# Optimization experiments

Hardware: AMD Instinct MI355X
Metric: run time of the kernel (lower is better)

## Reference

```python
import jax, jax.numpy as jnp
import numpy as np

C = 256            # in_channels
SHIFTS = (1, 2, 3, 4)
S = len(SHIFTS)
HID = C // S       # 64
H = W = 64
AREA = H * W
EPS = 1e-5
NORM_EPS = 1e-12
# offsets (dy, dx) encoded by the 8 one-hot 3x3 kernels (kernels 1..8)
OFFSETS = [(-1,-1), (-1,0), (-1,1), (0,1), (1,1), (1,0), (1,-1), (0,-1)]


def shift2d(x, dy, dx):
    # x: [b, c, H, W]; out[y, x] = x[y+dy, x+dx], zeros outside (== dilated depthwise conv with one-hot kernel)
    d = max(abs(dy), abs(dx), 1)
    xp = jnp.pad(x, ((0,0),(0,0),(d,d),(d,d)))
    return xp[:, :, d+dy:d+dy+x.shape[2], d+dx:d+dx+x.shape[3]]


def setup_inputs() -> dict:
    key = jax.random.key(0)
    ks = jax.random.split(key, 8)
    sd = 0.02
    return {
        "cen": jax.random.normal(ks[0], (4, C, H, W), dtype=jnp.float32),
        "query_w": jax.random.normal(ks[1], (S, HID, C), dtype=jnp.float32) * sd,
        "local_w": jax.random.normal(ks[2], (S, HID, C), dtype=jnp.float32) * sd,
        "key_w":   jax.random.normal(ks[3], (S, 8*HID, 8*C), dtype=jnp.float32) * sd,
        "value_w": jax.random.normal(ks[4], (S, 8*HID, 8*C), dtype=jnp.float32) * sd,
        "out_w":   jax.random.normal(ks[5], (C, C), dtype=jnp.float32) * sd,
        "bn_gamma": jnp.ones((C,), dtype=jnp.float32),
        "bn_beta":  jnp.zeros((C,), dtype=jnp.float32),
    }


def reference(cen, query_w, local_w, key_w, value_w, out_w, bn_gamma, bn_beta):
    b, _, h, w = cen.shape
    cenf = cen.reshape(b, C, AREA)
    keys, qs, vals, locs = [], [], [], []
    for i, d in enumerate(SHIFTS):
        # gather 8 dilated neighbors -> [b, 8C, area]
        surr = jnp.concatenate([shift2d(cen, dy*d, dx*d) for dy, dx in OFFSETS], axis=1)
        surr = surr.reshape(b, 8*C, AREA)
        keys.append(jnp.einsum('oc,bca->boa', key_w[i], surr))
        vals.append(jnp.einsum('oc,bca->boa', value_w[i], surr))
        qs.append(jnp.einsum('oc,bca->boa', query_w[i], cenf))
        locs.append(jnp.einsum('oc,bca->boa', local_w[i], cenf))
    keys = jnp.stack(keys, 1)   # [b,S,8h,area]
    vals = jnp.stack(vals, 1)   # [b,S,8h,area]
    qs   = jnp.stack(qs, 1)     # [b,S,h,area]
    locs = jnp.stack(locs, 1)   # [b,S,h,area]

    # L2 normalize over area (torch F.normalize: x / max(||x||, eps))
    kn = keys / jnp.maximum(jnp.linalg.norm(keys, axis=-1, keepdims=True), NORM_EPS)
    qn = qs   / jnp.maximum(jnp.linalg.norm(qs,   axis=-1, keepdims=True), NORM_EPS)

    # channel attention: contract over area -> [b,S,h,8h]
    score = jnp.einsum('bsha,bska->bshk', qn, kn)
    # InstanceNorm2d over (h, 8h) per (b, S), affine=False, biased var
    mu = score.mean(axis=(-2,-1), keepdims=True)
    var = score.var(axis=(-2,-1), keepdims=True)
    score = (score - mu) * jax.lax.rsqrt(var + EPS)
    ws = jax.nn.softmax(score, axis=-1)                     # [b,S,h,8h]
    wc = ws.reshape(b, S, HID, 8, HID).sum(axis=3)          # sum of 8 chunks -> [b,S,h,h]

    out = jnp.einsum('bshk,bska->bsha', ws, vals) - jnp.einsum('bshk,bska->bsha', wc, locs)
    out = out.reshape(b, C, h, w)

    # out_conv: 1x1 conv -> BatchNorm2d (training stats, biased var) -> ReLU
    out = jnp.einsum('oc,bchw->bohw', out_w, out)
    m = out.mean(axis=(0,2,3), keepdims=True)
    v = out.var(axis=(0,2,3), keepdims=True)
    out = (out - m) * jax.lax.rsqrt(v + EPS)
    out = out * bn_gamma[None, :, None, None] + bn_beta[None, :, None, None]
    return jax.nn.relu(out)
```

## Files before the change

kernel.cpp:

```cpp
#include <hip/hip_runtime.h>


typedef unsigned short u16;
typedef unsigned int u32;
typedef __attribute__((ext_vector_type(4))) unsigned int u32x4;
typedef __attribute__((ext_vector_type(8))) short s16x8;
typedef __attribute__((ext_vector_type(4))) float f32x4;

#define DEVFN static __device__ __forceinline__

DEVFN u16 f2bf(float f) {
    u32 u = __builtin_bit_cast(u32, f);
    u32 r = (u + 0x7fffu + ((u >> 16) & 1u)) >> 16;
    return (u16)r;
}
DEVFN float bf2f(u32 h) { u32 u = h << 16; return __builtin_bit_cast(float, u); }

typedef __attribute__((address_space(1))) const unsigned int gu32;
typedef __attribute__((address_space(3))) unsigned int lu32;
DEVFN void gld16(const void* g, void* l) {
    __builtin_amdgcn_global_load_lds((gu32*)g, (lu32*)l, 16, 0, 0);
}

__constant__ int cOFFY[8] = {-1,-1,-1, 0, 1, 1, 1, 0};
__constant__ int cOFFX[8] = {-1, 0, 1, 1, 1, 0,-1,-1};

DEVFN int swz(int r, int kb) { return r * 128 + (kb ^ ((r & 7) << 4)); }

template<int BM, int BN, int WRM, int WRN, int XG, int YG, int DM, int NRM>
__global__ __launch_bounds__(256, 2)
void gemm_tn(const u16* __restrict__ X, const u16* __restrict__ Y,
             void* __restrict__ D, const u16* __restrict__ cenT,
             const char* __restrict__ zeroPg, float* __restrict__ nrm,
             int K, int ldx, int ldy, int ldd, int sbits,
             long xb, long xs, long yb, long ys, long db, long dsn,
             long nb, long ns)
{
    const int tid  = threadIdx.x;
    const int lane = tid & 63;
    const int wid  = tid >> 6;
    const int z = blockIdx.z;
    const int b = z >> sbits;
    const int s = z & ((1 << sbits) - 1);
    const int m0 = blockIdx.x * BM;
    const int n0 = blockIdx.y * BN;
    const int dil = s + 1;
    const int wm0 = (wid >> 1) * (WRM * 16);
    const int wn0 = (wid & 1) * (WRN * 16);

    __shared__ __align__(16) char lds[2 * (BM + BN) * 128];

    const char* cenB = (const char*)(cenT + (long)b * (4096 * 256));
    const char* Xb = nullptr;
    const char* Yb = nullptr;
    if constexpr (!XG) Xb = (const char*)(X + b * xb + (long)s * xs + (long)m0 * ldx);
    if constexpr (!YG) Yb = (const char*)(Y + b * yb + (long)s * ys + (long)n0 * ldy);

    auto stage = [&](int bf, int t) {
        char* LX = lds + bf * ((BM + BN) * 128);
        char* LY = LX + BM * 128;
        if constexpr (!XG) {
            const char* base = Xb + (long)t * 128;
            #pragma unroll
            for (int r = 0; r < BM / 32; r++) {
                const int R = r * 32 + wid * 8 + (lane >> 3);
                gld16(base + (long)R * (ldx * 2) + (((lane & 7) * 16) ^ ((R & 7) << 4)),
                      LX + (r * 32 + wid * 8) * 128);
            }
        } else {
            const int j = t >> 2;
            const int dy = (j < 8) ? cOFFY[j] * dil : 0;
            const int dx = (j < 8) ? cOFFX[j] * dil : 0;
            const int cb = (t & 3) * 128;
            #pragma unroll
            for (int r = 0; r < BM / 32; r++) {
                const int R = r * 32 + wid * 8 + (lane >> 3);
                const int a = m0 + R, yy = (a >> 6) + dy, xx = (a & 63) + dx;
                const int off = ((lane & 7) * 16) ^ ((R & 7) << 4);
                const char* src = (((unsigned)yy < 64u) && ((unsigned)xx < 64u))
                    ? cenB + ((long)((yy << 6) + xx) << 9) + cb + off
                    : zeroPg + off;
                gld16(src, LX + (r * 32 + wid * 8) * 128);
            }
        }
        if constexpr (!YG) {
            const char* base = Yb + (long)t * 128;
            #pragma unroll
            for (int r = 0; r < BN / 32; r++) {
                const int R = r * 32 + wid * 8 + (lane >> 3);
                gld16(base + (long)R * (ldy * 2) + (((lane & 7) * 16) ^ ((R & 7) << 4)),
                      LY + (r * 32 + wid * 8) * 128);
            }
        } else {
            const int j = t >> 2;
            const int dy = (j < 8) ? cOFFY[j] * dil : 0;
            const int dx = (j < 8) ? cOFFX[j] * dil : 0;
            const int cb = (t & 3) * 128;
            #pragma unroll
            for (int r = 0; r < BN / 32; r++) {
                const int R = r * 32 + wid * 8 + (lane >> 3);
                const int a = n0 + R, yy = (a >> 6) + dy, xx = (a & 63) + dx;
                const int off = ((lane & 7) * 16) ^ ((R & 7) << 4);
                const char* src = (((unsigned)yy < 64u) && ((unsigned)xx < 64u))
                    ? cenB + ((long)((yy << 6) + xx) << 9) + cb + off
                    : zeroPg + off;
                gld16(src, LY + (r * 32 + wid * 8) * 128);
            }
        }
    };

    f32x4 acc[WRM][WRN] = {};

    auto comp = [&](int bf) {
        const char* LX = lds + bf * ((BM + BN) * 128);
        const char* LY = LX + BM * 128;
        #pragma unroll
        for (int kk = 0; kk < 2; kk++) {
            const int kb = kk * 64 + ((lane >> 4) << 4);
            s16x8 af[WRM], bfr[WRN];
            #pragma unroll
            for (int m = 0; m < WRM; m++)
                af[m] = *(const s16x8*)(LX + swz(wm0 + m * 16 + (lane & 15), kb));
            #pragma unroll
            for (int n = 0; n < WRN; n++)
                bfr[n] = *(const s16x8*)(LY + swz(wn0 + n * 16 + (lane & 15), kb));
            #pragma unroll
            for (int m = 0; m < WRM; m++)
                #pragma unroll
                for (int n = 0; n < WRN; n++)
                    acc[m][n] = __builtin_amdgcn_mfma_f32_16x16x32_bf16(af[m], bfr[n], acc[m][n], 0, 0, 0);
        }
    };

    const int nt = K / 64;
    stage(0, 0);
    __syncthreads();
    int cur = 0;
    for (int t = 0; t < nt; t++) {
        if (t + 1 < nt) stage(cur ^ 1, t + 1);
        comp(cur);
        __syncthreads();
        cur ^= 1;
    }

    if constexpr (NRM) {
        const int slot = (blockIdx.y << 1) + (wid & 1);
        #pragma unroll
        for (int m = 0; m < WRM; m++) {
            float ss[4] = {0.f, 0.f, 0.f, 0.f};
            float s1v[4] = {0.f, 0.f, 0.f, 0.f};
            #pragma unroll
            for (int n = 0; n < WRN; n++)
                #pragma unroll
                for (int i = 0; i < 4; i++) {
                    float v = (NRM == 1) ? bf2f(f2bf(acc[m][n][i])) : acc[m][n][i];
                    ss[i] += v * v;
                    if constexpr (NRM == 2) s1v[i] += v;
                }
            #pragma unroll
            for (int o = 1; o < 16; o <<= 1)
                #pragma unroll
                for (int i = 0; i < 4; i++) {
                    ss[i] += __shfl_xor(ss[i], o);
                    if constexpr (NRM == 2) s1v[i] += __shfl_xor(s1v[i], o);
                }
            if ((lane & 15) == 0) {
                const int row0 = m0 + wm0 + m * 16 + ((lane >> 4) << 2);
                #pragma unroll
                for (int i = 0; i < 4; i++) {
                    if constexpr (NRM == 1) {
                        nrm[((long)(b * nb + s * ns + row0 + i) << 6) + slot] = ss[i];
                    } else {
                        float* p = nrm + ((long)(row0 + i) << 8) + (b << 6) + slot;
                        p[0] = s1v[i];
                        p[65536] = ss[i];
                    }
                }
            }
        }
    }

    #pragma unroll
    for (int m = 0; m < WRM; m++) {
        const int row0 = m0 + wm0 + m * 16 + ((lane >> 4) << 2);
        #pragma unroll
        for (int n = 0; n < WRN; n++) {
            const int col = n0 + wn0 + n * 16 + (lane & 15);
            f32x4 a = acc[m][n];
            if constexpr (DM == 1) {
                float* Dp = (float*)D + b * db + (long)s * dsn;
                #pragma unroll
                for (int i = 0; i < 4; i++) Dp[(long)(row0 + i) * ldd + col] = a[i];
            } else {
                u16* Dp = (u16*)D + b * db + (long)s * dsn;
                #pragma unroll
                for (int i = 0; i < 4; i++) Dp[(long)(row0 + i) * ldd + col] = f2bf(a[i]);
            }
        }
    }
}

__global__ __launch_bounds__(256) void zero_f32(float* __restrict__ p, int n) {
    int i = blockIdx.x * 256 + threadIdx.x;
    if (i < n) p[i] = 0.f;
}

__global__ void castbf(const float* __restrict__ src, u16* __restrict__ dst, int n8, float scale) {
    int i = blockIdx.x * 256 + threadIdx.x;
    if (i >= n8) return;
    const float* s = src + (long)i * 8;
    u32x4 o;
    #pragma unroll
    for (int j = 0; j < 4; j++) {
        u16 lo = f2bf(s[2 * j] * scale), hi = f2bf(s[2 * j + 1] * scale);
        o[j] = (u32)lo | ((u32)hi << 16);
    }
    *(u32x4*)(dst + (long)i * 8) = o;
}

__global__ __launch_bounds__(256) void transpose_cast(const float* __restrict__ src, u16* __restrict__ dst,
                                                      int R, int C, float scale) {
    __shared__ float t[64][65];
    const int tx = threadIdx.x & 63, ty = threadIdx.x >> 6;
    const int c0 = blockIdx.x * 64, r0 = blockIdx.y * 64;
    const long bb = (long)blockIdx.z * R * C;
    const float* s = src + bb + (long)r0 * C + c0;
    #pragma unroll
    for (int i = 0; i < 16; i++) t[ty + i * 4][tx] = s[(long)(ty + i * 4) * C + tx];
    __syncthreads();
    u16* d = dst + bb + (long)c0 * R + r0;
    #pragma unroll
    for (int i = 0; i < 16; i++) d[(long)(ty + i * 4) * R + tx] = f2bf(t[tx][ty + i * 4] * scale);
}

__global__ __launch_bounds__(256) void softmax_in(const float* __restrict__ score,
                                                  const float* __restrict__ nQp,
                                                  const float* __restrict__ nKp,
                                                  u16* __restrict__ wswc) {
    const int bs = blockIdx.x, tid = threadIdx.x;
    const int b = bs >> 2, s = bs & 3;
    const float* S = score + (long)bs * 32768;
    __shared__ float invq[64], invk[512];
    if (tid < 64) {
        const float* p = nQp + ((long)(b * 256 + s * 64 + tid) << 6);
        float a = 0.f;
        #pragma unroll
        for (int j = 0; j < 64; j++) a += p[j];
        invq[tid] = 1.f / fmaxf(sqrtf(a), 1e-12f);
    }
    for (int i = tid; i < 512; i += 256) {
        const float* p = nKp + (((long)bs * 512 + i) << 6);
        float a = 0.f;
        #pragma unroll
        for (int j = 0; j < 64; j++) a += p[j];
        invk[i] = 1.f / fmaxf(sqrtf(a), 1e-12f);
    }
    __syncthreads();
    float s1 = 0.f, s2 = 0.f;
    for (int i = tid; i < 32768; i += 256) {
        float v = S[i] * invq[i >> 9] * invk[i & 511];
        s1 += v; s2 += v * v;
    }
    __shared__ float ra[256], rb[256];
    ra[tid] = s1; rb[tid] = s2; __syncthreads();
    for (int st = 128; st > 0; st >>= 1) {
        if (tid < st) { ra[tid] += ra[tid + st]; rb[tid] += rb[tid + st]; }
        __syncthreads();
    }
    const float mu = ra[0] * (1.f / 32768.f);
    const float var = rb[0] * (1.f / 32768.f) - mu * mu;
    const float rstd = rsqrtf(var + 1e-5f);
    const int wid = tid >> 6, lane = tid & 63;
    u16* W = wswc + (long)bs * 64 * 576;
    for (int r = wid; r < 64; r += 4) {
        float zv[8]; float mx = -3.0e38f;
        const float iq = invq[r];
        #pragma unroll
        for (int i = 0; i < 8; i++) {
            const int c = i * 64 + lane;
            zv[i] = (S[r * 512 + c] * iq * invk[c] - mu) * rstd;
            mx = fmaxf(mx, zv[i]);
        }
        #pragma unroll
        for (int o = 32; o > 0; o >>= 1) mx = fmaxf(mx, __shfl_xor(mx, o));
        float sum = 0.f;
        #pragma unroll
        for (int i = 0; i < 8; i++) { zv[i] = __expf(zv[i] - mx); sum += zv[i]; }
        #pragma unroll
        for (int o = 32; o > 0; o >>= 1) sum += __shfl_xor(sum, o);
        const float inv = 1.f / sum;
        float wcv = 0.f;
        #pragma unroll
        for (int i = 0; i < 8; i++) {
            float w = zv[i] * inv; wcv += w;
            W[r * 576 + i * 64 + lane] = f2bf(w);
        }
        W[r * 576 + 512 + lane] = f2bf(wcv);
    }
}

__global__ __launch_bounds__(256) void bn_finalize(const float* __restrict__ bnp,
                                                   const float* __restrict__ gamma,
                                                   const float* __restrict__ beta,
                                                   float* __restrict__ st) {
    const int c = threadIdx.x;
    const float* p = bnp + ((long)c << 8);
    float s1 = 0.f, s2 = 0.f;
    #pragma unroll 8
    for (int j = 0; j < 256; j++) { s1 += p[j]; s2 += p[65536 + j]; }
    const float mu = s1 * (1.f / 16384.f);
    const float var = s2 * (1.f / 16384.f) - mu * mu;
    const float g = gamma[c] * rsqrtf(var + 1e-5f);
    st[c * 2] = g;
    st[c * 2 + 1] = beta[c] - mu * g;
}

__global__ __launch_bounds__(256) void bn_apply(const u16* __restrict__ out2b,
                                                const float* __restrict__ st,
                                                float* __restrict__ out) {
    const long i8 = (long)blockIdx.x * 256 + threadIdx.x;
    const u32x4 v = *(const u32x4*)(out2b + i8 * 8);
    const int c = (int)((i8 * 8) >> 12) & 255;
    const float g = st[c * 2], bt = st[c * 2 + 1];
    float* o = out + i8 * 8;
    #pragma unroll
    for (int j = 0; j < 4; j++) {
        o[2 * j]     = fmaxf(bf2f(v[j] & 0xffff) * g + bt, 0.f);
        o[2 * j + 1] = fmaxf(bf2f(v[j] >> 16) * g + bt, 0.f);
    }
}

extern "C" void kernel_launch(void* const* d_in, const int* in_sizes, int n_in,
                              void* d_out, int out_size, void* d_ws, size_t ws_size,
                              hipStream_t stream) {
    (void)in_sizes; (void)n_in; (void)out_size; (void)ws_size;
    const float* cen   = (const float*)d_in[0];
    const float* qw    = (const float*)d_in[1];
    const float* lw    = (const float*)d_in[2];
    const float* kw    = (const float*)d_in[3];
    const float* vw    = (const float*)d_in[4];
    const float* ow    = (const float*)d_in[5];
    const float* gamma = (const float*)d_in[6];
    const float* beta  = (const float*)d_in[7];
    float* out = (float*)d_out;

    char* ws = (char*)d_ws;
    size_t off = 0;
    auto alloc = [&](size_t bytes) { size_t o = off; off += (bytes + 255) & ~(size_t)255; return o; };
    u16*   KWb   = (u16*)(ws + alloc(4L * 512 * 2048 * 2));
    u16*   VWt   = (u16*)(ws + alloc(4L * 2048 * 512 * 2));
    u16*   QWb   = (u16*)(ws + alloc(256L * 256 * 2));
    u16*   LWt   = (u16*)(ws + alloc(4L * 256 * 64 * 2));
    u16*   OWb   = (u16*)(ws + alloc(256L * 256 * 2));
    u16*   cenT  = (u16*)(ws + alloc(4L * 4096 * 256 * 2));
    u16*   keys  = (u16*)(ws + alloc(16L * 512 * 4096 * 2));
    u16*   qs    = (u16*)(ws + alloc(16L * 64 * 4096 * 2));
    float* score = (float*)(ws + alloc(16L * 64 * 512 * 4));
    u16*   WSWC  = (u16*)(ws + alloc(16L * 64 * 576 * 2));
    u16*   Xcomb = (u16*)(ws + alloc(16L * 64 * 2304 * 2));
    u16*   out1t = (u16*)(ws + alloc(4L * 4096 * 256 * 2));
    u16*   out2b = (u16*)(ws + alloc(4L * 256 * 4096 * 2));
    float* bnst  = (float*)(ws + alloc(256L * 2 * 4));
    char*  zpg   = (char*)(ws + alloc(256));
    float* nKp   = (float*)(ws + alloc(16L * 512 * 64 * 4));
    float* nQp   = (float*)(ws + alloc(4L * 256 * 64 * 4));
    float* bnp   = (float*)(ws + alloc(2L * 65536 * 4));

    zero_f32<<<dim3(1), 256, 0, stream>>>((float*)zpg, 64);
    castbf<<<dim3(2048), 256, 0, stream>>>(kw, KWb, 524288, 1.f);
    castbf<<<dim3(32),   256, 0, stream>>>(qw, QWb, 8192, 1.f);
    castbf<<<dim3(32),   256, 0, stream>>>(ow, OWb, 8192, 1.f);
    transpose_cast<<<dim3(32, 8, 4), 256, 0, stream>>>(vw, VWt, 512, 2048, 1.f);
    transpose_cast<<<dim3(4, 1, 4),  256, 0, stream>>>(lw, LWt, 64, 256, -1.f);
    transpose_cast<<<dim3(64, 4, 4), 256, 0, stream>>>(cen, cenT, 256, 4096, 1.f);

    gemm_tn<128,128,4,4, 0,1, 0, 1><<<dim3(4, 32, 16), 256, 0, stream>>>(
        KWb, nullptr, keys, cenT, zpg, nKp,
        2048, 2048, 0, 4096, 2,
        0L, 512L * 2048, 0L, 0L, 4L * 512 * 4096, 512L * 4096, 2048L, 512L);
    gemm_tn<128,128,4,4, 0,0, 0, 1><<<dim3(2, 32, 4), 256, 0, stream>>>(
        QWb, cenT, qs, cenT, zpg, nQp,
        256, 256, 256, 4096, 0,
        0L, 0L, 4096L * 256, 0L, 256L * 4096, 0L, 256L, 0L);
    gemm_tn<64,64,2,2, 0,0, 1, 0><<<dim3(1, 8, 16), 256, 0, stream>>>(
        qs, keys, score, cenT, zpg, nullptr,
        4096, 4096, 4096, 512, 2,
        256L * 4096, 64L * 4096, 4L * 512 * 4096, 512L * 4096, 4L * 64 * 512, 64L * 512, 0L, 0L);
    softmax_in<<<dim3(16), 256, 0, stream>>>(score, nQp, nKp, WSWC);

    gemm_tn<64,128,2,4, 0,0, 0, 0><<<dim3(1, 16, 16), 256, 0, stream>>>(
        WSWC, VWt, Xcomb, cenT, zpg, nullptr,
        512, 576, 512, 2304, 2,
        4L * 64 * 576, 64L * 576, 0L, 2048L * 512, 4L * 64 * 2304, 64L * 2304, 0L, 0L);
    gemm_tn<64,128,2,4, 0,0, 0, 0><<<dim3(1, 2, 16), 256, 0, stream>>>(
        WSWC + 512, LWt, Xcomb + 2048, cenT, zpg, nullptr,
        64, 576, 64, 2304, 2,
        4L * 64 * 576, 64L * 576, 0L, 256L * 64, 4L * 64 * 2304, 64L * 2304, 0L, 0L);
    gemm_tn<128,64,4,2, 1,0, 0, 0><<<dim3(32, 1, 16), 256, 0, stream>>>(
        nullptr, Xcomb, out1t, cenT, zpg, nullptr,
        2304, 0, 2304, 256, 2,
        0L, 0L, 4L * 64 * 2304, 64L * 2304, 4096L * 256, 64L, 0L, 0L);

    gemm_tn<128,128,4,4, 0,0, 0, 2><<<dim3(2, 32, 4), 256, 0, stream>>>(
        OWb, out1t, out2b, cenT, zpg, bnp,
        256, 256, 256, 4096, 0,
        0L, 0L, 4096L * 256, 0L, 256L * 4096, 0L, 0L, 0L);

    bn_finalize<<<dim3(1), 256, 0, stream>>>(bnp, gamma, beta, bnst);
    bn_apply<<<dim3(2048), 256, 0, stream>>>(out2b, bnst, out);
}
```

Baseline: 340.1 us.

## Add BK=32 tile path for key GEMM and split-K for score GEMM

Adds a BK=32 K-tile variant of the GEMM with its own LDS swizzle and launch bounds allowing four blocks per SM, and uses it for the large gathered key projection to raise occupancy. Adds split-K (4 slices) to the qs·keys score GEMM, which previously launched only 128 blocks over a 4096-long reduction. Each split writes its own partial plane, and the softmax kernel sums the four partials on load. This trades more partial-score traffic and a larger workspace for better GPU fill on the score GEMM. The K-loop also runs twice as many iterations with more syncs for the key GEMM.

```diff
diff --git a/kernel.cpp b/kernel.cpp
--- a/kernel.cpp
+++ b/kernel.cpp
@@ -27,15 +27,17 @@
 
 DEVFN int swz(int r, int kb) { return r * 128 + (kb ^ ((r & 7) << 4)); }
 
-template<int BM, int BN, int WRM, int WRN, int XG, int YG, int DM, int NRM>
-__global__ __launch_bounds__(256, 2)
+template<int BM, int BN, int WRM, int WRN, int XG, int YG, int DM, int NRM, int BK, int KSP>
+__global__ __launch_bounds__(256, (BK == 32 ? 4 : 2))
 void gemm_tn(const u16* __restrict__ X, const u16* __restrict__ Y,
              void* __restrict__ D, const u16* __restrict__ cenT,
              const char* __restrict__ zeroPg, float* __restrict__ nrm,
              int K, int ldx, int ldy, int ldd, int sbits,
              long xb, long xs, long yb, long ys, long db, long dsn,
-             long nb, long ns)
+             long nb, long ns, long kpl)
 {
+    static_assert(KSP == 1 || (!XG && !YG), "split-K only for non-gather");
+    constexpr int ROWB = BK * 2;
     const int tid  = threadIdx.x;
     const int lane = tid & 63;
     const int wid  = tid >> 6;
@@ -43,87 +45,149 @@
     const int b = z >> sbits;
     const int s = z & ((1 << sbits) - 1);
     const int m0 = blockIdx.x * BM;
-    const int n0 = blockIdx.y * BN;
+    const int ksl = (KSP > 1) ? ((int)blockIdx.y % KSP) : 0;
+    const int n0 = (KSP > 1 ? ((int)blockIdx.y / KSP) : (int)blockIdx.y) * BN;
+    const int koff = ksl * (K / KSP);
     const int dil = s + 1;
     const int wm0 = (wid >> 1) * (WRM * 16);
     const int wn0 = (wid & 1) * (WRN * 16);
 
-    __shared__ __align__(16) char lds[2 * (BM + BN) * 128];
+    __shared__ __align__(16) char lds[2 * (BM + BN) * ROWB];
 
     const char* cenB = (const char*)(cenT + (long)b * (4096 * 256));
     const char* Xb = nullptr;
     const char* Yb = nullptr;
-    if constexpr (!XG) Xb = (const char*)(X + b * xb + (long)s * xs + (long)m0 * ldx);
-    if constexpr (!YG) Yb = (const char*)(Y + b * yb + (long)s * ys + (long)n0 * ldy);
+    if constexpr (!XG) Xb = (const char*)(X + b * xb + (long)s * xs + (long)m0 * ldx + koff);
+    if constexpr (!YG) Yb = (const char*)(Y + b * yb + (long)s * ys + (long)n0 * ldy + koff);
 
     auto stage = [&](int bf, int t) {
-        char* LX = lds + bf * ((BM + BN) * 128);
-        char* LY = LX + BM * 128;
-        if constexpr (!XG) {
-            const char* base = Xb + (long)t * 128;
-            #pragma unroll
-            for (int r = 0; r < BM / 32; r++) {
-                const int R = r * 32 + wid * 8 + (lane >> 3);
-                gld16(base + (long)R * (ldx * 2) + (((lane & 7) * 16) ^ ((R & 7) << 4)),
-                      LX + (r * 32 + wid * 8) * 128);
+        char* LX = lds + bf * ((BM + BN) * ROWB);
+        char* LY = LX + BM * ROWB;
+        if constexpr (BK == 64) {
+            if constexpr (!XG) {
+                const char* base = Xb + (long)t * 128;
+                #pragma unroll
+                for (int r = 0; r < BM / 32; r++) {
+                    const int R = r * 32 + wid * 8 + (lane >> 3);
+                    gld16(base + (long)R * (ldx * 2) + (((lane & 7) * 16) ^ ((R & 7) << 4)),
+                          LX + (r * 32 + wid * 8) * 128);
+                }
+            } else {
+                const int j = t >> 2;
+                const int dy = (j < 8) ? cOFFY[j] * dil : 0;
+                const int dx = (j < 8) ? cOFFX[j] * dil : 0;
+                const int cb = (t & 3) * 128;
+                #pragma unroll
+                for (int r = 0; r < BM / 32; r++) {
+                    const int R = r * 32 + wid * 8 + (lane >> 3);
+                    const int a = m0 + R, yy = (a >> 6) + dy, xx = (a & 63) + dx;
+                    const int off = ((lane & 7) * 16) ^ ((R & 7) << 4);
+                    const char* src = (((unsigned)yy < 64u) && ((unsigned)xx < 64u))
+                        ? cenB + ((long)((yy << 6) + xx) << 9) + cb + off
+                        : zeroPg + off;
+                    gld16(src, LX + (r * 32 + wid * 8) * 128);
+                }
+            }
+            if constexpr (!YG) {
+                const char* base = Yb + (long)t * 128;
+                #pragma unroll
+                for (int r = 0; r < BN / 32; r++) {
+                    const int R = r * 32 + wid * 8 + (lane >> 3);
+                    gld16(base + (long)R * (ldy * 2) + (((lane & 7) * 16) ^ ((R & 7) << 4)),
+                          LY + (r * 32 + wid * 8) * 128);
+                }
+            } else {
+                const int j = t >> 2;
+                const int dy = (j < 8) ? cOFFY[j] * dil : 0;
+                const int dx = (j < 8) ? cOFFX[j] * dil : 0;
+                const int cb = (t & 3) * 128;
+                #pragma unroll
+                for (int r = 0; r < BN / 32; r++) {
+                    const int R = r * 32 + wid * 8 + (lane >> 3);
+                    const int a = n0 + R, yy = (a >> 6) + dy, xx = (a & 63) + dx;
+                    const int off = ((lane & 7) * 16) ^ ((R & 7) << 4);
+                    const char* src = (((unsigned)yy < 64u) && ((unsigned)xx < 64u))
+                        ? cenB + ((long)((yy << 6) + xx) << 9) + cb + off
+                        : zeroPg + off;
+                    gld16(src, LY + (r * 32 + wid * 8) * 128);
+                }
             }
         } else {
-            const int j = t >> 2;
+            const int kc = (((tid & 3) ^ ((tid >> 3) & 3)) << 4);
+            const int j = t >> 3;
             const int dy = (j < 8) ? cOFFY[j] * dil : 0;
             const int dx = (j < 8) ? cOFFX[j] * dil : 0;
-            const int cb = (t & 3) * 128;
-            #pragma unroll
-            for (int r = 0; r < BM / 32; r++) {
-                const int R = r * 32 + wid * 8 + (lane >> 3);
-                const int a = m0 + R, yy = (a >> 6) + dy, xx = (a & 63) + dx;
-                const int off = ((lane & 7) * 16) ^ ((R & 7) << 4);
-                const char* src = (((unsigned)yy < 64u) && ((unsigned)xx < 64u))
-                    ? cenB + ((long)((yy << 6) + xx) << 9) + cb + off
-                    : zeroPg + off;
-                gld16(src, LX + (r * 32 + wid * 8) * 128);
-            }
-        }
-        if constexpr (!YG) {
-            const char* base = Yb + (long)t * 128;
-            #pragma unroll
-            for (int r = 0; r < BN / 32; r++) {
-                const int R = r * 32 + wid * 8 + (lane >> 3);
-                gld16(base + (long)R * (ldy * 2) + (((lane & 7) * 16) ^ ((R & 7) << 4)),
-                      LY + (r * 32 + wid * 8) * 128);
+            const int cb = (t & 7) * 64;
+            if constexpr (!XG) {
+                const char* base = Xb + (long)t * 64;
+                #pragma unroll
+                for (int r = 0; r < BM / 64; r++) {
+                    const int R = r * 64 + (tid >> 2);
+                    gld16(base + (long)R * (ldx * 2) + kc, LX + (r * 64 + (tid >> 2)) * 64);
+                }
+            } else {
+                #pragma unroll
+                for (int r = 0; r < BM / 64; r++) {
+                    const int R = r * 64 + (tid >> 2);
+                    const int a = m0 + R, yy = (a >> 6) + dy, xx = (a & 63) + dx;
+                    const char* src = (((unsigned)yy < 64u) && ((unsigned)xx < 64u))
+                        ? cenB + ((long)((yy << 6) + xx) << 9) + cb + kc
+                        : zeroPg + kc;
+                    gld16(src, LX + (r * 64 + (tid >> 2)) * 64);
+                }
+            }
+            if constexpr (!YG) {
+                const char* base = Yb + (long)t * 64;
+                #pragma unroll
+                for (int r = 0; r < BN / 64; r++) {
+                    const int R = r * 64 + (tid >> 2);
+                    gld16(base + (long)R * (ldy * 2) + kc, LY + (r * 64 + (tid >> 2)) * 64);
+                }
+            } else {
+                #pragma unroll
+                for (int r = 0; r < BN / 64; r++) {
+                    const int R = r * 64 + (tid >> 2);
+                    const int a = n0 + R, yy = (a >> 6) + dy, xx = (a & 63) + dx;
+                    const char* src = (((unsigned)yy < 64u) && ((unsigned)xx < 64u))
+                        ? cenB + ((long)((yy << 6) + xx) << 9) + cb + kc
+                        : zeroPg + kc;
+                    gld16(src, LY + (r * 64 + (tid >> 2)) * 64);
+                }
+            }
+        }
+    };
+
+    f32x4 acc[WRM][WRN] = {};
+
+    auto comp = [&](int bf) {
+        const char* LX = lds + bf * ((BM + BN) * ROWB);
+        const char* LY = LX + BM * ROWB;
+        if constexpr (BK == 64) {
+            #pragma unroll
+            for (int kk = 0; kk < 2; kk++) {
+                const int kb = kk * 64 + ((lane >> 4) << 4);
+                s16x8 af[WRM], bfr[WRN];
+                #pragma unroll
+                for (int m = 0; m < WRM; m++)
+                    af[m] = *(const s16x8*)(LX + swz(wm0 + m * 16 + (lane & 15), kb));
+                #pragma unroll
+                for (int n = 0; n < WRN; n++)
+                    bfr[n] = *(const s16x8*)(LY + swz(wn0 + n * 16 + (lane & 15), kb));
+                #pragma unroll
+                for (int m = 0; m < WRM; m++)
+                    #pragma unroll
+                    for (int n = 0; n < WRN; n++)
+                        acc[m][n] = __builtin_amdgcn_mfma_f32_16x16x32_bf16(af[m], bfr[n], acc[m][n], 0, 0, 0);
             }
         } else {
-            const int j = t >> 2;
-            const int dy = (j < 8) ? cOFFY[j] * dil : 0;
-            const int dx = (j < 8) ? cOFFX[j] * dil : 0;
-            const int cb = (t & 3) * 128;
-            #pragma unroll
-            for (int r = 0; r < BN / 32; r++) {
-                const int R = r * 32 + wid * 8 + (lane >> 3);
-                const int a = n0 + R, yy = (a >> 6) + dy, xx = (a & 63) + dx;
-                const int off = ((lane & 7) * 16) ^ ((R & 7) << 4);
-                const char* src = (((unsigned)yy < 64u) && ((unsigned)xx < 64u))
-                    ? cenB + ((long)((yy << 6) + xx) << 9) + cb + off
-                    : zeroPg + off;
-                gld16(src, LY + (r * 32 + wid * 8) * 128);
-            }
-        }
-    };
-
-    f32x4 acc[WRM][WRN] = {};
-
-    auto comp = [&](int bf) {
-        const char* LX = lds + bf * ((BM + BN) * 128);
-        const char* LY = LX + BM * 128;
-        #pragma unroll
-        for (int kk = 0; kk < 2; kk++) {
-            const int kb = kk * 64 + ((lane >> 4) << 4);
+            const int fk = (((lane >> 4) ^ ((lane >> 1) & 3)) << 4);
             s16x8 af[WRM], bfr[WRN];
             #pragma unroll
             for (int m = 0; m < WRM; m++)
-                af[m] = *(const s16x8*)(LX + swz(wm0 + m * 16 + (lane & 15), kb));
+                af[m] = *(const s16x8*)(LX + (wm0 + m * 16 + (lane & 15)) * 64 + fk);
             #pragma unroll
             for (int n = 0; n < WRN; n++)
-                bfr[n] = *(const s16x8*)(LY + swz(wn0 + n * 16 + (lane & 15), kb));
+                bfr[n] = *(const s16x8*)(LY + (wn0 + n * 16 + (lane & 15)) * 64 + fk);
             #pragma unroll
             for (int m = 0; m < WRM; m++)
                 #pragma unroll
@@ -132,7 +196,7 @@
         }
     };
 
-    const int nt = K / 64;
+    const int nt = (K / KSP) / BK;
     stage(0, 0);
     __syncthreads();
     int cur = 0;
@@ -144,7 +208,7 @@
     }
 
     if constexpr (NRM) {
-        const int slot = (blockIdx.y << 1) + (wid & 1);
+        const int slot = ((int)blockIdx.y << 1) + (wid & 1);
         #pragma unroll
         for (int m = 0; m < WRM; m++) {
             float ss[4] = {0.f, 0.f, 0.f, 0.f};
@@ -188,7 +252,7 @@
             const int col = n0 + wn0 + n * 16 + (lane & 15);
             f32x4 a = acc[m][n];
             if constexpr (DM == 1) {
-                float* Dp = (float*)D + b * db + (long)s * dsn;
+                float* Dp = (float*)D + (long)ksl * kpl + b * db + (long)s * dsn;
                 #pragma unroll
                 for (int i = 0; i < 4; i++) Dp[(long)(row0 + i) * ldd + col] = a[i];
             } else {
@@ -237,6 +301,7 @@
                                                   const float* __restrict__ nQp,
                                                   const float* __restrict__ nKp,
                                                   u16* __restrict__ wswc) {
+    constexpr long PL = 524288;
     const int bs = blockIdx.x, tid = threadIdx.x;
     const int b = bs >> 2, s = bs & 3;
     const float* S = score + (long)bs * 32768;
@@ -256,9 +321,12 @@
         invk[i] = 1.f / fmaxf(sqrtf(a), 1e-12f);
     }
     __syncthreads();
+    auto ldS = [&](int i) -> float {
+        return S[i] + S[i + PL] + S[i + 2 * PL] + S[i + 3 * PL];
+    };
     float s1 = 0.f, s2 = 0.f;
     for (int i = tid; i < 32768; i += 256) {
-        float v = S[i] * invq[i >> 9] * invk[i & 511];
+        float v = ldS(i) * invq[i >> 9] * invk[i & 511];
         s1 += v; s2 += v * v;
     }
     __shared__ float ra[256], rb[256];
@@ -278,7 +346,7 @@
         #pragma unroll
         for (int i = 0; i < 8; i++) {
             const int c = i * 64 + lane;
-            zv[i] = (S[r * 512 + c] * iq * invk[c] - mu) * rstd;
+            zv[i] = (ldS(r * 512 + c) * iq * invk[c] - mu) * rstd;
             mx = fmaxf(mx, zv[i]);
         }
         #pragma unroll
@@ -355,7 +423,7 @@
     u16*   cenT  = (u16*)(ws + alloc(4L * 4096 * 256 * 2));
     u16*   keys  = (u16*)(ws + alloc(16L * 512 * 4096 * 2));
     u16*   qs    = (u16*)(ws + alloc(16L * 64 * 4096 * 2));
-    float* score = (float*)(ws + alloc(16L * 64 * 512 * 4));
+    float* score = (float*)(ws + alloc(4L * 16 * 64 * 512 * 4));
     u16*   WSWC  = (u16*)(ws + alloc(16L * 64 * 576 * 2));
     u16*   Xcomb = (u16*)(ws + alloc(16L * 64 * 2304 * 2));
     u16*   out1t = (u16*)(ws + alloc(4L * 4096 * 256 * 2));
@@ -374,37 +442,38 @@
     transpose_cast<<<dim3(4, 1, 4),  256, 0, stream>>>(lw, LWt, 64, 256, -1.f);
     transpose_cast<<<dim3(64, 4, 4), 256, 0, stream>>>(cen, cenT, 256, 4096, 1.f);
 
-    gemm_tn<128,128,4,4, 0,1, 0, 1><<<dim3(4, 32, 16), 256, 0, stream>>>(
+    gemm_tn<128,128,4,4, 0,1, 0, 1, 32, 1><<<dim3(4, 32, 16), 256, 0, stream>>>(
         KWb, nullptr, keys, cenT, zpg, nKp,
         2048, 2048, 0, 4096, 2,
-        0L, 512L * 2048, 0L, 0L, 4L * 512 * 4096, 512L * 4096, 2048L, 512L);
-    gemm_tn<128,128,4,4, 0,0, 0, 1><<<dim3(2, 32, 4), 256, 0, stream>>>(
+        0L, 512L * 2048, 0L, 0L, 4L * 512 * 4096, 512L * 4096, 2048L, 512L, 0L);
+    gemm_tn<128,128,4,4, 0,0, 0, 1, 64, 1><<<dim3(2, 32, 4), 256, 0, stream>>>(
         QWb, cenT, qs, cenT, zpg, nQp,
         256, 256, 256, 4096, 0,
-        0L, 0L, 4096L * 256, 0L, 256L * 4096, 0L, 256L, 0L);
-    gemm_tn<64,64,2,2, 0,0, 1, 0><<<dim3(1, 8, 16), 256, 0, stream>>>(
+        0L, 0L, 4096L * 256, 0L, 256L * 4096, 0L, 256L, 0L, 0L);
+    gemm_tn<64,64,2,2, 0,0, 1, 0, 64, 4><<<dim3(1, 32, 16), 256, 0, stream>>>(
         qs, keys, score, cenT, zpg, nullptr,
         4096, 4096, 4096, 512, 2,
-        256L * 4096, 64L * 4096, 4L * 512 * 4096, 512L * 4096, 4L * 64 * 512, 64L * 512, 0L, 0L);
+        256L * 4096, 64L * 4096, 4L * 512 * 4096, 512L * 4096, 4L * 64 * 512, 64L * 512,
+        0L, 0L, 524288L);
     softmax_in<<<dim3(16), 256, 0, stream>>>(score, nQp, nKp, WSWC);
 
-    gemm_tn<64,128,2,4, 0,0, 0, 0><<<dim3(1, 16, 16), 256, 0, stream>>>(
+    gemm_tn<64,128,2,4, 0,0, 0, 0, 64, 1><<<dim3(1, 16, 16), 256, 0, stream>>>(
         WSWC, VWt, Xcomb, cenT, zpg, nullptr,
         512, 576, 512, 2304, 2,
-        4L * 64 * 576, 64L * 576, 0L, 2048L * 512, 4L * 64 * 2304, 64L * 2304, 0L, 0L);
-    gemm_tn<64,128,2,4, 0,0, 0, 0><<<dim3(1, 2, 16), 256, 0, stream>>>(
+        4L * 64 * 576, 64L * 576, 0L, 2048L * 512, 4L * 64 * 2304, 64L * 2304, 0L, 0L, 0L);
+    gemm_tn<64,128,2,4, 0,0, 0, 0, 64, 1><<<dim3(1, 2, 16), 256, 0, stream>>>(
         WSWC + 512, LWt, Xcomb + 2048, cenT, zpg, nullptr,
         64, 576, 64, 2304, 2,
-        4L * 64 * 576, 64L * 576, 0L, 256L * 64, 4L * 64 * 2304, 64L * 2304, 0L, 0L);
-    gemm_tn<128,64,4,2, 1,0, 0, 0><<<dim3(32, 1, 16), 256, 0, stream>>>(
+        4L * 64 * 576, 64L * 576, 0L, 256L * 64, 4L * 64 * 2304, 64L * 2304, 0L, 0L, 0L);
+    gemm_tn<128,64,4,2, 1,0, 0, 0, 64, 1><<<dim3(32, 1, 16), 256, 0, stream>>>(
         nullptr, Xcomb, out1t, cenT, zpg, nullptr,
         2304, 0, 2304, 256, 2,
-        0L, 0L, 4L * 64 * 2304, 64L * 2304, 4096L * 256, 64L, 0L, 0L);
-
-    gemm_tn<128,128,4,4, 0,0, 0, 2><<<dim3(2, 32, 4), 256, 0, stream>>>(
+        0L, 0L, 4L * 64 * 2304, 64L * 2304, 4096L * 256, 64L, 0L, 0L, 0L);
+
+    gemm_tn<128,128,4,4, 0,0, 0, 2, 64, 1><<<dim3(2, 32, 4), 256, 0, stream>>>(
         OWb, out1t, out2b, cenT, zpg, bnp,
         256, 256, 256, 4096, 0,
-        0L, 0L, 4096L * 256, 0L, 256L * 4096, 0L, 0L, 0L);
+        0L, 0L, 4096L * 256, 0L, 256L * 4096, 0L, 0L, 0L, 0L);
 
     bn_finalize<<<dim3(1), 256, 0, stream>>>(bnp, gamma, beta, bnst);
     bn_apply<<<dim3(2048), 256, 0, stream>>>(out2b, bnst, out);
```

New measurement: 352.4 us. 1.04x slower.

## Split-K the score GEMM and remap workgroups for XCD locality

Applied to the files above, without the earlier changes.

Adds a split-K template parameter. The q·k score GEMM (K=4096, previously only 128 workgroups) now runs as 4 K-slices into separate fp32 partial planes, which the softmax/instance-norm kernel sums on load. It also adds an optional workgroup-index swizzle, enabled on the two gather GEMMs, so that consecutive tiles map to the same XCD for better L2 reuse. In exchange the score buffer grows fourfold and softmax reads four times the data, but the score GEMM gets more parallelism on the GPU.

```diff
diff --git a/kernel.cpp b/kernel.cpp
--- a/kernel.cpp
+++ b/kernel.cpp
@@ -27,23 +27,33 @@
 
 DEVFN int swz(int r, int kb) { return r * 128 + (kb ^ ((r & 7) << 4)); }
 
-template<int BM, int BN, int WRM, int WRN, int XG, int YG, int DM, int NRM>
+template<int BM, int BN, int WRM, int WRN, int XG, int YG, int DM, int NRM, int KSP, int SWZ>
 __global__ __launch_bounds__(256, 2)
 void gemm_tn(const u16* __restrict__ X, const u16* __restrict__ Y,
              void* __restrict__ D, const u16* __restrict__ cenT,
              const char* __restrict__ zeroPg, float* __restrict__ nrm,
              int K, int ldx, int ldy, int ldd, int sbits,
              long xb, long xs, long yb, long ys, long db, long dsn,
-             long nb, long ns)
+             long nb, long ns, long kpl)
 {
+    static_assert(KSP == 1 || (!XG && !YG), "split-K only for non-gather");
+    int bx = blockIdx.x, by = blockIdx.y, bz = blockIdx.z;
+    if constexpr (SWZ) {
+        const int gx = gridDim.x, gy = gridDim.y;
+        const int nwg = gx * gy * (int)gridDim.z;
+        const int flat = bx + gx * (by + gy * bz);
+        const int r = (flat & 7) * (nwg >> 3) + (flat >> 3);
+        bx = r % gx; by = (r / gx) % gy; bz = r / (gx * gy);
+    }
     const int tid  = threadIdx.x;
     const int lane = tid & 63;
     const int wid  = tid >> 6;
-    const int z = blockIdx.z;
-    const int b = z >> sbits;
-    const int s = z & ((1 << sbits) - 1);
-    const int m0 = blockIdx.x * BM;
-    const int n0 = blockIdx.y * BN;
+    const int b = bz >> sbits;
+    const int s = bz & ((1 << sbits) - 1);
+    const int m0 = bx * BM;
+    const int ksl = (KSP > 1) ? (by % KSP) : 0;
+    const int n0 = (KSP > 1 ? (by / KSP) : by) * BN;
+    const int koff = ksl * (K / KSP);
     const int dil = s + 1;
     const int wm0 = (wid >> 1) * (WRM * 16);
     const int wn0 = (wid & 1) * (WRN * 16);
@@ -53,8 +63,8 @@
     const char* cenB = (const char*)(cenT + (long)b * (4096 * 256));
     const char* Xb = nullptr;
     const char* Yb = nullptr;
-    if constexpr (!XG) Xb = (const char*)(X + b * xb + (long)s * xs + (long)m0 * ldx);
-    if constexpr (!YG) Yb = (const char*)(Y + b * yb + (long)s * ys + (long)n0 * ldy);
+    if constexpr (!XG) Xb = (const char*)(X + b * xb + (long)s * xs + (long)m0 * ldx + koff);
+    if constexpr (!YG) Yb = (const char*)(Y + b * yb + (long)s * ys + (long)n0 * ldy + koff);
 
     auto stage = [&](int bf, int t) {
         char* LX = lds + bf * ((BM + BN) * 128);
@@ -132,7 +142,7 @@
         }
     };
 
-    const int nt = K / 64;
+    const int nt = (K / KSP) / 64;
     stage(0, 0);
     __syncthreads();
     int cur = 0;
@@ -144,7 +154,7 @@
     }
 
     if constexpr (NRM) {
-        const int slot = (blockIdx.y << 1) + (wid & 1);
+        const int slot = (by << 1) + (wid & 1);
         #pragma unroll
         for (int m = 0; m < WRM; m++) {
             float ss[4] = {0.f, 0.f, 0.f, 0.f};
@@ -188,7 +198,7 @@
             const int col = n0 + wn0 + n * 16 + (lane & 15);
             f32x4 a = acc[m][n];
             if constexpr (DM == 1) {
-                float* Dp = (float*)D + b * db + (long)s * dsn;
+                float* Dp = (float*)D + (long)ksl * kpl + b * db + (long)s * dsn;
                 #pragma unroll
                 for (int i = 0; i < 4; i++) Dp[(long)(row0 + i) * ldd + col] = a[i];
             } else {
@@ -237,6 +247,7 @@
                                                   const float* __restrict__ nQp,
                                                   const float* __restrict__ nKp,
                                                   u16* __restrict__ wswc) {
+    constexpr long PL = 524288;
     const int bs = blockIdx.x, tid = threadIdx.x;
     const int b = bs >> 2, s = bs & 3;
     const float* S = score + (long)bs * 32768;
@@ -256,9 +267,12 @@
         invk[i] = 1.f / fmaxf(sqrtf(a), 1e-12f);
     }
     __syncthreads();
+    auto ldS = [&](int i) -> float {
+        return S[i] + S[i + PL] + S[i + 2 * PL] + S[i + 3 * PL];
+    };
     float s1 = 0.f, s2 = 0.f;
     for (int i = tid; i < 32768; i += 256) {
-        float v = S[i] * invq[i >> 9] * invk[i & 511];
+        float v = ldS(i) * invq[i >> 9] * invk[i & 511];
         s1 += v; s2 += v * v;
     }
     __shared__ float ra[256], rb[256];
@@ -278,7 +292,7 @@
         #pragma unroll
         for (int i = 0; i < 8; i++) {
             const int c = i * 64 + lane;
-            zv[i] = (S[r * 512 + c] * iq * invk[c] - mu) * rstd;
+            zv[i] = (ldS(r * 512 + c) * iq * invk[c] - mu) * rstd;
             mx = fmaxf(mx, zv[i]);
         }
         #pragma unroll
@@ -355,7 +369,7 @@
     u16*   cenT  = (u16*)(ws + alloc(4L * 4096 * 256 * 2));
     u16*   keys  = (u16*)(ws + alloc(16L * 512 * 4096 * 2));
     u16*   qs    = (u16*)(ws + alloc(16L * 64 * 4096 * 2));
-    float* score = (float*)(ws + alloc(16L * 64 * 512 * 4));
+    float* score = (float*)(ws + alloc(4L * 16 * 64 * 512 * 4));
     u16*   WSWC  = (u16*)(ws + alloc(16L * 64 * 576 * 2));
     u16*   Xcomb = (u16*)(ws + alloc(16L * 64 * 2304 * 2));
     u16*   out1t = (u16*)(ws + alloc(4L * 4096 * 256 * 2));
@@ -374,37 +388,38 @@
     transpose_cast<<<dim3(4, 1, 4),  256, 0, stream>>>(lw, LWt, 64, 256, -1.f);
     transpose_cast<<<dim3(64, 4, 4), 256, 0, stream>>>(cen, cenT, 256, 4096, 1.f);
 
-    gemm_tn<128,128,4,4, 0,1, 0, 1><<<dim3(4, 32, 16), 256, 0, stream>>>(
+    gemm_tn<128,128,4,4, 0,1, 0, 1, 1, 1><<<dim3(4, 32, 16), 256, 0, stream>>>(
         KWb, nullptr, keys, cenT, zpg, nKp,
         2048, 2048, 0, 4096, 2,
-        0L, 512L * 2048, 0L, 0L, 4L * 512 * 4096, 512L * 4096, 2048L, 512L);
-    gemm_tn<128,128,4,4, 0,0, 0, 1><<<dim3(2, 32, 4), 256, 0, stream>>>(
+        0L, 512L * 2048, 0L, 0L, 4L * 512 * 4096, 512L * 4096, 2048L, 512L, 0L);
+    gemm_tn<128,128,4,4, 0,0, 0, 1, 1, 0><<<dim3(2, 32, 4), 256, 0, stream>>>(
         QWb, cenT, qs, cenT, zpg, nQp,
         256, 256, 256, 4096, 0,
-        0L, 0L, 4096L * 256, 0L, 256L * 4096, 0L, 256L, 0L);
-    gemm_tn<64,64,2,2, 0,0, 1, 0><<<dim3(1, 8, 16), 256, 0, stream>>>(
+        0L, 0L, 4096L * 256, 0L, 256L * 4096, 0L, 256L, 0L, 0L);
+    gemm_tn<64,64,2,2, 0,0, 1, 0, 4, 0><<<dim3(1, 32, 16), 256, 0, stream>>>(
         qs, keys, score, cenT, zpg, nullptr,
         4096, 4096, 4096, 512, 2,
-        256L * 4096, 64L * 4096, 4L * 512 * 4096, 512L * 4096, 4L * 64 * 512, 64L * 512, 0L, 0L);
+        256L * 4096, 64L * 4096, 4L * 512 * 4096, 512L * 4096, 4L * 64 * 512, 64L * 512,
+        0L, 0L, 524288L);
     softmax_in<<<dim3(16), 256, 0, stream>>>(score, nQp, nKp, WSWC);
 
-    gemm_tn<64,128,2,4, 0,0, 0, 0><<<dim3(1, 16, 16), 256, 0, stream>>>(
+    gemm_tn<64,128,2,4, 0,0, 0, 0, 1, 0><<<dim3(1, 16, 16), 256, 0, stream>>>(
         WSWC, VWt, Xcomb, cenT, zpg, nullptr,
         512, 576, 512, 2304, 2,
-        4L * 64 * 576, 64L * 576, 0L, 2048L * 512, 4L * 64 * 2304, 64L * 2304, 0L, 0L);
-    gemm_tn<64,128,2,4, 0,0, 0, 0><<<dim3(1, 2, 16), 256, 0, stream>>>(
+        4L * 64 * 576, 64L * 576, 0L, 2048L * 512, 4L * 64 * 2304, 64L * 2304, 0L, 0L, 0L);
+    gemm_tn<64,128,2,4, 0,0, 0, 0, 1, 0><<<dim3(1, 2, 16), 256, 0, stream>>>(
         WSWC + 512, LWt, Xcomb + 2048, cenT, zpg, nullptr,
         64, 576, 64, 2304, 2,
-        4L * 64 * 576, 64L * 576, 0L, 256L * 64, 4L * 64 * 2304, 64L * 2304, 0L, 0L);
-    gemm_tn<128,64,4,2, 1,0, 0, 0><<<dim3(32, 1, 16), 256, 0, stream>>>(
+        4L * 64 * 576, 64L * 576, 0L, 256L * 64, 4L * 64 * 2304, 64L * 2304, 0L, 0L, 0L);
+    gemm_tn<128,64,4,2, 1,0, 0, 0, 1, 1><<<dim3(32, 1, 16), 256, 0, stream>>>(
         nullptr, Xcomb, out1t, cenT, zpg, nullptr,
         2304, 0, 2304, 256, 2,
-        0L, 0L, 4L * 64 * 2304, 64L * 2304, 4096L * 256, 64L, 0L, 0L);
-
-    gemm_tn<128,128,4,4, 0,0, 0, 2><<<dim3(2, 32, 4), 256, 0, stream>>>(
+        0L, 0L, 4L * 64 * 2304, 64L * 2304, 4096L * 256, 64L, 0L, 0L, 0L);
+
+    gemm_tn<128,128,4,4, 0,0, 0, 2, 1, 0><<<dim3(2, 32, 4), 256, 0, stream>>>(
         OWb, out1t, out2b, cenT, zpg, bnp,
         256, 256, 256, 4096, 0,
-        0L, 0L, 4096L * 256, 0L, 256L * 4096, 0L, 0L, 0L);
+        0L, 0L, 4096L * 256, 0L, 256L * 4096, 0L, 0L, 0L, 0L);
 
     bn_finalize<<<dim3(1), 256, 0, stream>>>(bnp, gamma, beta, bnst);
     bn_apply<<<dim3(2048), 256, 0, stream>>>(out2b, bnst, out);
```

New measurement: 334.6 us. No clear change (-1.6%).
